# Kernel tuning notes

Hardware: AMD Instinct MI355X
Metric: run time of the kernel (lower is better)

## Reference

```python
import jax, jax.numpy as jnp
import numpy as np

# module hyperparameters (match init_kwargs)
IN_PLANES = 64
OUT = 64            # out_planes
N_HASHES = 4
CHUNK = 25          # chunk_size
GROUPS = 8
KS = 56             # kernel_size == attended axis length H
GP = OUT // GROUPS  # group_planes = 8
EPS_N = 5e-5        # F.normalize eps
BN_EPS = 1e-5
F_GW, F_GV1, F_GV2 = 0.1, 0.1, 1.0


def l2norm(x, axis):
    # torch F.normalize(p=2, eps=EPS_N)
    n = jnp.sqrt(jnp.sum(x * x, axis=axis, keepdims=True))
    return x / jnp.maximum(n, EPS_N)


def setup_inputs() -> dict:
    key = jax.random.key(0)
    k1, k2, k3, k4 = jax.random.split(key, 4)
    x = jax.random.normal(k1, (2, IN_PLANES, KS, 56), jnp.float32)
    conv_w = jax.random.normal(k2, (OUT * 3 // 2, IN_PLANES), jnp.float32) * np.float32(np.sqrt(1.0 / IN_PLANES))
    bn_gamma = jnp.ones((OUT * 3 // 2,), jnp.float32)
    bn_beta = jnp.zeros((OUT * 3 // 2,), jnp.float32)
    relative = jax.random.normal(k3, (KS, GP * 3 // 2), jnp.float32) * np.float32(np.sqrt(1.0 / GP))
    # LSH random rotations: hash_buckets = min(56//25 + (56//25)%2, 10) = 2 -> hb//2 = 1
    rotations = jax.random.normal(k4, (OUT // 2, N_HASHES, 1), jnp.float32)
    return dict(x=x, conv_w=conv_w, bn_gamma=bn_gamma, bn_beta=bn_beta,
                relative=relative, rotations=rotations)


def reference(x, conv_w, bn_gamma, bn_beta, relative, rotations):
    # width=False: (N,C,H,W) -> (N,W,C,H), flatten batch with W
    N, C, Hax, W = x.shape
    x = jnp.transpose(x, (0, 3, 1, 2)).reshape(N * W, C, Hax)
    B, H = N * W, Hax
    hash_buckets = min(H // CHUNK + (H // CHUNK) % 2, 10)

    # 1x1 conv + eval-mode BatchNorm (running_mean=0, running_var=1)
    qkv = jnp.einsum('oc,bch->boh', conv_w, x)
    qkv = qkv / np.float32(np.sqrt(1.0 + BN_EPS)) * bn_gamma[None, :, None] + bn_beta[None, :, None]
    # NOTE: original uses raw reshape (B,C3,H) -> (B,H,C3), NOT a transpose
    qkv = qkv.reshape(B, H, OUT * 3 // 2)
    w_match = qkv[..., :OUT // 2]   # (B,H,out/2)
    v_match = qkv[..., OUT // 2:]   # (B,H,out)
    w_emb = relative[:, :GP // 2]
    v_emb = relative[:, GP // 2:]

    # LSH hashing (rotations shared across batch)
    rot = jnp.einsum('btf,fhi->bhti', w_match, rotations)
    rot = jnp.concatenate([rot, -rot], axis=-1)           # (B,nh,H,hash_buckets)
    codes = jnp.argmax(rot, axis=-1)
    codes = codes + (jnp.arange(N_HASHES) * hash_buckets)[None, :, None]
    codes = codes.reshape(B, N_HASHES * H)

    indices = jnp.argsort(codes, axis=-1)                 # stable sort into buckets
    undo = jnp.argsort(indices, axis=-1)
    mod = indices % H
    w_s = jnp.take_along_axis(w_match, mod[:, :, None], axis=1)
    v_s = jnp.take_along_axis(v_match, mod[:, :, None], axis=1)

    padding = (CHUNK - H % CHUNK) % CHUNK                 # 19 here
    w_b = w_s.reshape(B, N_HASHES, H, OUT // 2)
    v_b = v_s.reshape(B, N_HASHES, H, OUT)
    if padding:
        w_b = jnp.concatenate([w_b, w_b[:, :, -padding:, :]], axis=2)
        v_b = jnp.concatenate([v_b, v_b[:, :, -padding:, :]], axis=2)
        w_emb = jnp.concatenate([w_emb, w_emb[-padding:, :]], axis=0)
        v_emb = jnp.concatenate([v_emb, v_emb[-padding:, :]], axis=0)
    # raw reshapes, exactly as torch does (groups folded via flat reshape)
    w_b = w_b.reshape(B, GROUPS, N_HASHES, -1, CHUNK, GP // 2)
    v_b = v_b.reshape(B, GROUPS, N_HASHES, -1, CHUNK, GP)
    w_emb = w_emb.reshape(-1, CHUNK, GP // 2)             # (K,25,4)
    v_emb = v_emb.reshape(-1, CHUNK, GP)                  # (K,25,8)
    K = w_emb.shape[0]

    def adj(t):  # look-around over the chunk axis (dim 3), cat on dim 4
        return jnp.concatenate([t, jnp.roll(t, 1, axis=3), jnp.roll(t, -1, axis=3)], axis=4)

    def adj_emb(t):
        return jnp.concatenate([t, jnp.roll(t, 1, axis=0), jnp.roll(t, -1, axis=0)], axis=1)

    w_m = adj(l2norm(w_b, -1))
    v_a = adj(v_b)
    w_e = adj_emb(w_emb)
    v_e = adj_emb(v_emb)

    raw = jnp.einsum('bghkie,bghkje->bghkij', w_b, w_m)            # (B,g,h,K,25,75)
    emb_sc = F_GW * jnp.einsum('bghkie,kje->bghkij', w_b, w_e)
    ss = jnp.concatenate([raw, emb_sc], axis=1)                    # (B,2g,h,K,25,75)
    ss = l2norm(ss, 1).reshape(B, 2, GROUPS, N_HASHES, K, CHUNK, CHUNK * 3).sum(axis=1)

    bs = jax.nn.logsumexp(ss, axis=-1, keepdims=True)
    score = jnp.exp(ss - bs)
    bs = bs.reshape(B, GROUPS, N_HASHES, K * CHUNK)

    r_out = F_GV2 * jnp.einsum('bgukij,bgukje->bgukie', score, v_a)
    r_emb = F_GV1 * jnp.einsum('bgukij,kje->bgukie', score, v_e)
    ret = jnp.concatenate([r_out, r_emb], axis=-1)                 # (B,g,h,K,25,2*gp)
    ret = ret.reshape(B, N_HASHES, K, CHUNK, OUT * 2)              # raw reshape
    ret = ret.reshape(B, OUT * 2, N_HASHES, K, CHUNK)              # raw reshape
    ret = l2norm(ret, 1).reshape(B, N_HASHES, K, CHUNK, OUT, 2).sum(axis=-1)
    bs = l2norm(bs, 1).sum(axis=1)                                 # (B,h,K*25)

    ret = ret.reshape(B, N_HASHES, K * CHUNK, OUT)
    if padding:
        ret = ret[:, :, :-padding, :]
        bs = bs[:, :, :-padding]
    ret = ret.reshape(B, N_HASHES * H, OUT)
    bs = bs.reshape(B, N_HASHES * H)

    ret = jnp.take_along_axis(ret, undo[:, :, None], axis=1)      # unsort
    bs = jnp.take_along_axis(bs, undo, axis=1)
    ret = ret.reshape(B, N_HASHES, H, OUT)
    bs = bs.reshape(B, N_HASHES, H, 1)

    probs = jax.nn.softmax(bs, axis=1)
    ret = jnp.sum(ret * probs, axis=1)                             # (B,H,out)
    ret = ret.reshape(N, W, H, OUT)
    return jnp.transpose(ret, (0, 3, 2, 1))                        # (N,out,H,W)
```

## Files before the change

kernel.cpp:

```cpp
#include <hip/hip_runtime.h>
#include <math.h>


#define EPSN 5e-5f
#define INV_EPSN 20000.0f
#define LOG2E 1.4426950408889634f
#define LN2   0.6931471805599453f

__device__ __forceinline__ float dot4(const float4 a, const float4 b) {
    return a.x * b.x + a.y * b.y + a.z * b.z + a.w * b.w;
}
__device__ __forceinline__ void fma4(float4& a, float s, const float4 v) {
    a.x += s * v.x; a.y += s * v.y; a.z += s * v.z; a.w += s * v.w;
}

__global__ __launch_bounds__(256) void k0_xT(
        const float* __restrict__ x, float* __restrict__ xT) {
    __shared__ float T[64][57];
    const int n = blockIdx.x, h = blockIdx.y, tid = threadIdx.x;
    const float* xb = x + n * 200704 + h * 56;
    #pragma unroll 7
    for (int i = tid; i < 3584; i += 256) {
        int c = i / 56, w = i % 56;
        T[c][w] = xb[c * 3136 + w];
    }
    __syncthreads();
    float* xo = xT + n * 200704 + h * 3584;
    #pragma unroll 7
    for (int i = tid; i < 3584; i += 256) {
        int w = i / 64, c = i % 64;
        xo[w * 64 + c] = T[c][w];
    }
}

__global__ __launch_bounds__(256) void k12_qkv_sort(
        const float* __restrict__ xT, const float* __restrict__ cw,
        const float* __restrict__ gamma, const float* __restrict__ beta,
        const float* __restrict__ rot, float* __restrict__ qkv,
        int* __restrict__ idx_buf) {
    __shared__ float xsT[56 * 68];
    __shared__ float cws[96 * 64];
    __shared__ float wm[56 * 32];
    __shared__ float rl[128];
    __shared__ float gs[96], bt[96];
    __shared__ int code[224];
    __shared__ int srt[224];
    const int b = blockIdx.x, n = b / 56, w = b % 56, tid = threadIdx.x;
    const float* xTb = xT + n * 200704 + w * 64;
    #pragma unroll 4
    for (int i = tid; i < 896; i += 256) {
        int h = i / 16, cq = i % 16;
        *(float4*)&xsT[h * 68 + cq * 4] =
            *(const float4*)&xTb[h * 3584 + cq * 4];
    }
    #pragma unroll 8
    for (int i = tid; i < 6144; i += 256) cws[i] = cw[i];
    if (tid < 128) rl[tid] = rot[tid];
    if (tid < 96) { gs[tid] = gamma[tid]; bt[tid] = beta[tid]; }
    __syncthreads();
    const float inv_s = 1.0f / sqrtf(1.0f + 1.0e-5f);
    for (int tl = tid; tl < 1344; tl += 256) {
        int oq = tl / 56, h = tl % 56;
        int o0 = oq * 4;
        float s0 = 0.f, s1 = 0.f, s2 = 0.f, s3 = 0.f;
        #pragma unroll
        for (int cs = 0; cs < 16; ++cs) {
            float4 xv = *(const float4*)&xsT[h * 68 + cs * 4];
            float4 c0 = *(const float4*)&cws[(o0 + 0) * 64 + cs * 4];
            float4 c1 = *(const float4*)&cws[(o0 + 1) * 64 + cs * 4];
            float4 c2 = *(const float4*)&cws[(o0 + 2) * 64 + cs * 4];
            float4 c3 = *(const float4*)&cws[(o0 + 3) * 64 + cs * 4];
            s0 += dot4(xv, c0); s1 += dot4(xv, c1);
            s2 += dot4(xv, c2); s3 += dot4(xv, c3);
        }
        #pragma unroll
        for (int qq = 0; qq < 4; ++qq) {
            int o = o0 + qq;
            float sv = (qq == 0) ? s0 : (qq == 1) ? s1 : (qq == 2) ? s2 : s3;
            float val = sv * inv_s * gs[o] + bt[o];
            int j = o * 56 + h;
            qkv[b * 5376 + j] = val;
            int f = j % 96;
            if (f < 32) wm[(j / 96) * 32 + f] = val;
        }
    }
    __syncthreads();
    if (tid < 224) {
        int u = tid / 56, t = tid % 56;
        float s = 0.f;
        #pragma unroll 8
        for (int f = 0; f < 32; ++f) s += wm[t * 32 + f] * rl[f * 4 + u];
        code[tid] = ((s < 0.f) ? 1 : 0) + 2 * u;
    }
    __syncthreads();
    if (tid < 224) {
        int c = code[tid], r = 0;
        #pragma unroll 8
        for (int p = 0; p < 224; ++p) {
            int cp = code[p];
            r += (int)((cp < c) | ((cp == c) & (p < tid)));
        }
        srt[r] = tid;
    }
    __syncthreads();
    if (tid < 224) idx_buf[b * 224 + tid] = srt[tid];
}

__global__ __launch_bounds__(256) void k3_attn(
        const float* __restrict__ qkv, const int* __restrict__ idx_buf,
        const float* __restrict__ rel, float* __restrict__ Rb,
        float* __restrict__ bsb) {
    __shared__ __align__(16) float Wc[8][3][25][4];
    __shared__ __align__(16) float Vb[8][3][25][8];
    __shared__ __align__(16) float WbK[8][25][4];
    __shared__ float DIT[75][25];
    __shared__ int ibL[224];
    const int b = blockIdx.x, u = blockIdx.y, k = blockIdx.z;
    const int tid = threadIdx.x;
    const float* q = qkv + b * 5376;

    if (tid < 224) ibL[tid] = idx_buf[b * 224 + tid];
    __syncthreads();

    #pragma unroll 3
    for (int idx = tid; idx < 600; idx += 256) {
        int i = idx % 25, kk = (idx / 25) % 3, g = idx / 75;
        int p0 = 1200 * g + 300 * u + 100 * kk + 4 * i;
        int h = p0 / 2400, r = p0 % 2400, t = r >> 5, f = r & 31;
        int row = (t < 56) ? t : t - 19;
        int tt = ibL[h * 56 + row] % 56;
        float4 v = *(const float4*)&q[tt * 96 + f];
        if (kk == k) *(float4*)&WbK[g][i][0] = v;
        float ni = fminf(__builtin_amdgcn_rsqf(dot4(v, v)), INV_EPSN);
        v.x *= ni; v.y *= ni; v.z *= ni; v.w *= ni;
        *(float4*)&Wc[g][kk][i][0] = v;
    }
    #pragma unroll 5
    for (int idx = tid; idx < 1200; idx += 256) {
        int half = idx & 1, fr = idx >> 1;
        int i = fr % 25, kk = (fr / 25) % 3, g = fr / 75;
        int p0 = 2400 * g + 600 * u + 200 * kk + 8 * i + 4 * half;
        int h = p0 / 4800, r = p0 % 4800, t = r >> 6, f = r & 63;
        int row = (t < 56) ? t : t - 19;
        int tt = ibL[h * 56 + row] % 56;
        *(float4*)&Vb[g][kk][i][4 * half] = *(const float4*)&q[tt * 96 + 32 + f];
    }
    __syncthreads();

    if (tid < 250) {
        const int i = tid % 25, jg = tid / 25;
        float4 wb8[8];
        #pragma unroll
        for (int g = 0; g < 8; ++g) wb8[g] = *(const float4*)&WbK[g][i][0];
        #pragma unroll
        for (int it = 0; it < 8; ++it) {
            int j = jg * 8 + it;
            if (j < 75) {
                int ks = j / 25, jj = j % 25;
                int roww = (j < 56) ? j : j - 19;
                float4 we = *(const float4*)&rel[roww * 12];
                we.x *= 0.1f; we.y *= 0.1f; we.z *= 0.1f; we.w *= 0.1f;
                float s2 = 0.f;
                #pragma unroll
                for (int g = 0; g < 8; ++g) {
                    float4 wcn = *(const float4*)&Wc[g][ks][jj][0];
                    float raw = dot4(wb8[g], wcn);
                    float emb = dot4(wb8[g], we);
                    s2 += raw * raw + emb * emb;
                }
                DIT[j][i] = fminf(__builtin_amdgcn_rsqf(s2), INV_EPSN);
            }
        }
    }
    __syncthreads();

    #pragma unroll 3
    for (int idx = tid; idx < 600; idx += 256) {
        int i = idx % 25, kk = (idx / 25) % 3, g = idx / 75;
        int tw = kk * 25 + i;
        int roww = (tw < 56) ? tw : tw - 19;
        float4 we = *(const float4*)&rel[roww * 12];
        float4 v = *(const float4*)&Wc[g][kk][i][0];
        v.x += 0.1f * we.x; v.y += 0.1f * we.y;
        v.z += 0.1f * we.z; v.w += 0.1f * we.w;
        *(float4*)&Wc[g][kk][i][0] = v;
    }
    __syncthreads();

    if (tid < 200) {
        const int g = tid & 7, i = tid >> 3;
        const float4 wbr = *(const float4*)&WbK[g][i][0];
        float se = 0.f;
        float4 a0 = {0,0,0,0}, a1 = {0,0,0,0}, a2 = {0,0,0,0}, a3 = {0,0,0,0};
        #pragma unroll
        for (int ks = 0; ks < 3; ++ks) {
            #pragma unroll
            for (int jj = 0; jj < 25; ++jj) {
                const int jP = ks * 25 + jj;
                const int roww = (jP < 56) ? jP : jP - 19;
                float di = DIT[jP][i];
                float e = __builtin_amdgcn_exp2f(
                    dot4(wbr, *(const float4*)&Wc[g][ks][jj][0]) * di * LOG2E);
                se += e;
                const float4* vv = (const float4*)&Vb[g][ks][jj][0];
                fma4(a0, e, vv[0]); fma4(a1, e, vv[1]);
                float4 ve0 = *(const float4*)&rel[roww * 12 + 4];
                float4 ve1 = *(const float4*)&rel[roww * 12 + 8];
                fma4(a2, e, ve0); fma4(a3, e, ve1);
            }
        }
        bsb[b * 2400 + g * 300 + u * 75 + k * 25 + i] =
            __builtin_amdgcn_logf(se) * LN2;
        const float rinv = 1.0f / se;
        const float r2 = 0.1f * rinv;
        a0.x *= rinv; a0.y *= rinv; a0.z *= rinv; a0.w *= rinv;
        a1.x *= rinv; a1.y *= rinv; a1.z *= rinv; a1.w *= rinv;
        a2.x *= r2;   a2.y *= r2;   a2.z *= r2;   a2.w *= r2;
        a3.x *= r2;   a3.y *= r2;   a3.z *= r2;   a3.w *= r2;
        float* rp = Rb + b * 38400 + 4800 * g + 1200 * u + 400 * k + 16 * i;
        ((float4*)rp)[0] = a0;
        ((float4*)rp)[1] = a1;
        ((float4*)rp)[2] = a2;
        ((float4*)rp)[3] = a3;
    }
}

__global__ __launch_bounds__(512) void k45_post(
        const float* __restrict__ Rb, const float* __restrict__ bsb,
        const int* __restrict__ idx_buf, float* __restrict__ out) {
    __shared__ float D[300];
    __shared__ float bsn[300];
    __shared__ float retU[224][32];
    __shared__ float bsU[224];
    __shared__ int idxL[224];
    const int b = blockIdx.x, oh = blockIdx.y, tid = threadIdx.x;
    const int n = b / 56, w = b % 56, o0 = oh * 32;
    const float* R = Rb + b * 38400;
    if (tid < 224) idxL[tid] = idx_buf[b * 224 + tid];
    if (tid < 300) {
        float s = 0.f;
        #pragma unroll 16
        for (int c = 0; c < 128; ++c) { float v = R[c * 300 + tid]; s += v * v; }
        D[tid] = fminf(__builtin_amdgcn_rsqf(s), INV_EPSN);
    }
    if (tid >= 512 - 300 + 88) { }
    if (tid < 300) {
        int u = tid / 75, t = tid % 75;
        float s2 = 0.f, sum = 0.f;
        #pragma unroll
        for (int g = 0; g < 8; ++g) {
            float v = bsb[b * 2400 + g * 300 + u * 75 + t];
            s2 += v * v; sum += v;
        }
        bsn[tid] = sum / fmaxf(sqrtf(s2), EPSN);
    }
    __syncthreads();
    if (tid < 224) {
        int u3 = tid / 56, t = tid % 56;
        bsU[idxL[tid]] = bsn[u3 * 75 + t];
    }
    #pragma unroll 4
    for (int idx = tid; idx < 224 * 32; idx += 512) {
        int p = idx >> 5, oc = idx & 31;
        int o = o0 + oc;
        int u3 = p / 56, t = p % 56;
        int k3 = t / 25, i3 = t % 25;
        int q0 = 9600 * u3 + 3200 * k3 + 128 * i3 + 2 * o;
        float2 rv = *(const float2*)&R[q0];
        int r0 = q0 % 300;
        float val = rv.x * D[r0] + rv.y * D[r0 + 1];
        retU[idxL[p]][oc] = val;
    }
    __syncthreads();
    for (int idx = tid; idx < 56 * 32; idx += 512) {
        int h = idx >> 5, oc = idx & 31;
        int o = o0 + oc;
        float b0 = bsU[h], b1 = bsU[56 + h], b2 = bsU[112 + h], b3 = bsU[168 + h];
        float m = fmaxf(fmaxf(b0, b1), fmaxf(b2, b3));
        float e0 = __builtin_amdgcn_exp2f((b0 - m) * LOG2E);
        float e1 = __builtin_amdgcn_exp2f((b1 - m) * LOG2E);
        float e2 = __builtin_amdgcn_exp2f((b2 - m) * LOG2E);
        float e3 = __builtin_amdgcn_exp2f((b3 - m) * LOG2E);
        float ps = e0 + e1 + e2 + e3;
        float val = (retU[h][oc] * e0 + retU[56 + h][oc] * e1 +
                     retU[112 + h][oc] * e2 + retU[168 + h][oc] * e3) / ps;
        out[((n * 64 + o) * 56 + h) * 56 + w] = val;
    }
}

extern "C" void kernel_launch(void* const* d_in, const int* in_sizes, int n_in,
                              void* d_out, int out_size, void* d_ws, size_t ws_size,
                              hipStream_t stream) {
    (void)in_sizes; (void)n_in; (void)out_size; (void)ws_size;
    const float* x     = (const float*)d_in[0];
    const float* cw    = (const float*)d_in[1];
    const float* gamma = (const float*)d_in[2];
    const float* beta  = (const float*)d_in[3];
    const float* rel   = (const float*)d_in[4];
    const float* rot   = (const float*)d_in[5];
    float* ws  = (float*)d_ws;
    float* qkv = ws;
    float* bsb = ws + 602112;
    float* Rb  = ws + 870912;
    float* xT  = Rb;
    int*   idx = (int*)(ws + 5171712);

    k0_xT<<<dim3(2, 56), 256, 0, stream>>>(x, xT);
    k12_qkv_sort<<<112, 256, 0, stream>>>(xT, cw, gamma, beta, rot, qkv, idx);
    k3_attn<<<dim3(112, 4, 3), 256, 0, stream>>>(qkv, idx, rel, Rb, bsb);
    k45_post<<<dim3(112, 2), 512, 0, stream>>>(Rb, bsb, idx, (float*)d_out);
}
```

Before: 150.7 us.

## Widen attention kernel to 512 threads, split key loop across lane pairs

The attention kernel now runs 512 threads per block. The score loop is split so each pair of lanes covers alternating keys, and the partial sums are combined with xor-shuffles. The relative-embedding table is staged in shared memory instead of being read repeatedly from global memory, and LOG2E is folded into the stored inverse norms. This adds parallelism to the latency-bound exp/accumulate phase, at the cost of shuffle reductions and more register pressure per block under the larger launch bound.

```diff
diff --git a/kernel.cpp b/kernel.cpp
--- a/kernel.cpp
+++ b/kernel.cpp
@@ -106,7 +106,7 @@
     if (tid < 224) idx_buf[b * 224 + tid] = srt[tid];
 }
 
-__global__ __launch_bounds__(256) void k3_attn(
+__global__ __launch_bounds__(512) void k3_attn(
         const float* __restrict__ qkv, const int* __restrict__ idx_buf,
         const float* __restrict__ rel, float* __restrict__ Rb,
         float* __restrict__ bsb) {
@@ -114,16 +114,18 @@
     __shared__ __align__(16) float Vb[8][3][25][8];
     __shared__ __align__(16) float WbK[8][25][4];
     __shared__ float DIT[75][25];
+    __shared__ __align__(16) float relL[672];
     __shared__ int ibL[224];
     const int b = blockIdx.x, u = blockIdx.y, k = blockIdx.z;
     const int tid = threadIdx.x;
     const float* q = qkv + b * 5376;
 
     if (tid < 224) ibL[tid] = idx_buf[b * 224 + tid];
-    __syncthreads();
-
-    #pragma unroll 3
-    for (int idx = tid; idx < 600; idx += 256) {
+    for (int i2 = tid; i2 < 672; i2 += 512) relL[i2] = rel[i2];
+    __syncthreads();
+
+    #pragma unroll 2
+    for (int idx = tid; idx < 600; idx += 512) {
         int i = idx % 25, kk = (idx / 25) % 3, g = idx / 75;
         int p0 = 1200 * g + 300 * u + 100 * kk + 4 * i;
         int h = p0 / 2400, r = p0 % 2400, t = r >> 5, f = r & 31;
@@ -135,8 +137,8 @@
         v.x *= ni; v.y *= ni; v.z *= ni; v.w *= ni;
         *(float4*)&Wc[g][kk][i][0] = v;
     }
-    #pragma unroll 5
-    for (int idx = tid; idx < 1200; idx += 256) {
+    #pragma unroll 3
+    for (int idx = tid; idx < 1200; idx += 512) {
         int half = idx & 1, fr = idx >> 1;
         int i = fr % 25, kk = (fr / 25) % 3, g = fr / 75;
         int p0 = 2400 * g + 600 * u + 200 * kk + 8 * i + 4 * half;
@@ -147,39 +149,37 @@
     }
     __syncthreads();
 
-    if (tid < 250) {
+    if (tid < 375) {
         const int i = tid % 25, jg = tid / 25;
         float4 wb8[8];
         #pragma unroll
         for (int g = 0; g < 8; ++g) wb8[g] = *(const float4*)&WbK[g][i][0];
         #pragma unroll
-        for (int it = 0; it < 8; ++it) {
-            int j = jg * 8 + it;
-            if (j < 75) {
-                int ks = j / 25, jj = j % 25;
-                int roww = (j < 56) ? j : j - 19;
-                float4 we = *(const float4*)&rel[roww * 12];
-                we.x *= 0.1f; we.y *= 0.1f; we.z *= 0.1f; we.w *= 0.1f;
-                float s2 = 0.f;
-                #pragma unroll
-                for (int g = 0; g < 8; ++g) {
-                    float4 wcn = *(const float4*)&Wc[g][ks][jj][0];
-                    float raw = dot4(wb8[g], wcn);
-                    float emb = dot4(wb8[g], we);
-                    s2 += raw * raw + emb * emb;
-                }
-                DIT[j][i] = fminf(__builtin_amdgcn_rsqf(s2), INV_EPSN);
+        for (int it = 0; it < 5; ++it) {
+            int j = jg * 5 + it;
+            int ks = (j >= 25) + (j >= 50), jj = j - ks * 25;
+            int roww = (j < 56) ? j : j - 19;
+            float4 we = *(const float4*)&relL[roww * 12];
+            we.x *= 0.1f; we.y *= 0.1f; we.z *= 0.1f; we.w *= 0.1f;
+            float s2 = 0.f;
+            #pragma unroll
+            for (int g = 0; g < 8; ++g) {
+                float4 wcn = *(const float4*)&Wc[g][ks][jj][0];
+                float raw = dot4(wb8[g], wcn);
+                float emb = dot4(wb8[g], we);
+                s2 += raw * raw + emb * emb;
             }
-        }
-    }
-    __syncthreads();
-
-    #pragma unroll 3
-    for (int idx = tid; idx < 600; idx += 256) {
+            DIT[j][i] = fminf(__builtin_amdgcn_rsqf(s2), INV_EPSN) * LOG2E;
+        }
+    }
+    __syncthreads();
+
+    #pragma unroll 2
+    for (int idx = tid; idx < 600; idx += 512) {
         int i = idx % 25, kk = (idx / 25) % 3, g = idx / 75;
         int tw = kk * 25 + i;
         int roww = (tw < 56) ? tw : tw - 19;
-        float4 we = *(const float4*)&rel[roww * 12];
+        float4 we = *(const float4*)&relL[roww * 12];
         float4 v = *(const float4*)&Wc[g][kk][i][0];
         v.x += 0.1f * we.x; v.y += 0.1f * we.y;
         v.z += 0.1f * we.z; v.w += 0.1f * we.w;
@@ -187,41 +187,52 @@
     }
     __syncthreads();
 
-    if (tid < 200) {
-        const int g = tid & 7, i = tid >> 3;
+    if (tid < 400) {
+        const int half = tid & 1, gi = tid >> 1;
+        const int g = gi & 7, i = gi >> 3;
         const float4 wbr = *(const float4*)&WbK[g][i][0];
         float se = 0.f;
         float4 a0 = {0,0,0,0}, a1 = {0,0,0,0}, a2 = {0,0,0,0}, a3 = {0,0,0,0};
-        #pragma unroll
-        for (int ks = 0; ks < 3; ++ks) {
-            #pragma unroll
-            for (int jj = 0; jj < 25; ++jj) {
-                const int jP = ks * 25 + jj;
-                const int roww = (jP < 56) ? jP : jP - 19;
-                float di = DIT[jP][i];
+        #pragma unroll 4
+        for (int jt = 0; jt < 38; ++jt) {
+            int j = jt * 2 + half;
+            if (j < 75) {
+                int ks = (j >= 25) + (j >= 50), jj = j - ks * 25;
+                int roww = (j < 56) ? j : j - 19;
                 float e = __builtin_amdgcn_exp2f(
-                    dot4(wbr, *(const float4*)&Wc[g][ks][jj][0]) * di * LOG2E);
+                    dot4(wbr, *(const float4*)&Wc[g][ks][jj][0]) * DIT[j][i]);
                 se += e;
                 const float4* vv = (const float4*)&Vb[g][ks][jj][0];
                 fma4(a0, e, vv[0]); fma4(a1, e, vv[1]);
-                float4 ve0 = *(const float4*)&rel[roww * 12 + 4];
-                float4 ve1 = *(const float4*)&rel[roww * 12 + 8];
+                float4 ve0 = *(const float4*)&relL[roww * 12 + 4];
+                float4 ve1 = *(const float4*)&relL[roww * 12 + 8];
                 fma4(a2, e, ve0); fma4(a3, e, ve1);
             }
         }
-        bsb[b * 2400 + g * 300 + u * 75 + k * 25 + i] =
-            __builtin_amdgcn_logf(se) * LN2;
-        const float rinv = 1.0f / se;
-        const float r2 = 0.1f * rinv;
-        a0.x *= rinv; a0.y *= rinv; a0.z *= rinv; a0.w *= rinv;
-        a1.x *= rinv; a1.y *= rinv; a1.z *= rinv; a1.w *= rinv;
-        a2.x *= r2;   a2.y *= r2;   a2.z *= r2;   a2.w *= r2;
-        a3.x *= r2;   a3.y *= r2;   a3.z *= r2;   a3.w *= r2;
-        float* rp = Rb + b * 38400 + 4800 * g + 1200 * u + 400 * k + 16 * i;
-        ((float4*)rp)[0] = a0;
-        ((float4*)rp)[1] = a1;
-        ((float4*)rp)[2] = a2;
-        ((float4*)rp)[3] = a3;
+        se += __shfl_xor(se, 1);
+        a0.x += __shfl_xor(a0.x, 1); a0.y += __shfl_xor(a0.y, 1);
+        a0.z += __shfl_xor(a0.z, 1); a0.w += __shfl_xor(a0.w, 1);
+        a1.x += __shfl_xor(a1.x, 1); a1.y += __shfl_xor(a1.y, 1);
+        a1.z += __shfl_xor(a1.z, 1); a1.w += __shfl_xor(a1.w, 1);
+        a2.x += __shfl_xor(a2.x, 1); a2.y += __shfl_xor(a2.y, 1);
+        a2.z += __shfl_xor(a2.z, 1); a2.w += __shfl_xor(a2.w, 1);
+        a3.x += __shfl_xor(a3.x, 1); a3.y += __shfl_xor(a3.y, 1);
+        a3.z += __shfl_xor(a3.z, 1); a3.w += __shfl_xor(a3.w, 1);
+        if (half == 0) {
+            bsb[b * 2400 + g * 300 + u * 75 + k * 25 + i] =
+                __builtin_amdgcn_logf(se) * LN2;
+            const float rinv = 1.0f / se;
+            const float r2 = 0.1f * rinv;
+            a0.x *= rinv; a0.y *= rinv; a0.z *= rinv; a0.w *= rinv;
+            a1.x *= rinv; a1.y *= rinv; a1.z *= rinv; a1.w *= rinv;
+            a2.x *= r2;   a2.y *= r2;   a2.z *= r2;   a2.w *= r2;
+            a3.x *= r2;   a3.y *= r2;   a3.z *= r2;   a3.w *= r2;
+            float* rp = Rb + b * 38400 + 4800 * g + 1200 * u + 400 * k + 16 * i;
+            ((float4*)rp)[0] = a0;
+            ((float4*)rp)[1] = a1;
+            ((float4*)rp)[2] = a2;
+            ((float4*)rp)[3] = a3;
+        }
     }
 }
 
@@ -243,7 +254,6 @@
         for (int c = 0; c < 128; ++c) { float v = R[c * 300 + tid]; s += v * v; }
         D[tid] = fminf(__builtin_amdgcn_rsqf(s), INV_EPSN);
     }
-    if (tid >= 512 - 300 + 88) { }
     if (tid < 300) {
         int u = tid / 75, t = tid % 75;
         float s2 = 0.f, sum = 0.f;
@@ -307,6 +317,6 @@
 
     k0_xT<<<dim3(2, 56), 256, 0, stream>>>(x, xT);
     k12_qkv_sort<<<112, 256, 0, stream>>>(xT, cw, gamma, beta, rot, qkv, idx);
-    k3_attn<<<dim3(112, 4, 3), 256, 0, stream>>>(qkv, idx, rel, Rb, bsb);
+    k3_attn<<<dim3(112, 4, 3), 512, 0, stream>>>(qkv, idx, rel, Rb, bsb);
     k45_post<<<dim3(112, 2), 512, 0, stream>>>(Rb, bsb, idx, (float*)d_out);
 }
```

New measurement: 140.9 us. 1.07x faster.
